# Kernel optimization log

Measured on AMD Instinct MI355X. Metric: run time of the kernel, lower is better.

## Reference

```python
import jax, jax.numpy as jnp
import numpy as np

DIM = 1024
HEADS = 16
DIM_HEAD = 64
SCALE = DIM_HEAD ** -0.5
LN_EPS = 1e-5


def layer_norm(x, g, b):
    mu = jnp.mean(x, axis=-1, keepdims=True)
    var = jnp.mean(jnp.square(x - mu), axis=-1, keepdims=True)
    return (x - mu) * jax.lax.rsqrt(var + LN_EPS) * g + b


def setup_inputs() -> dict:
    key = jax.random.key(0)
    ks = jax.random.split(key, 8)
    w_std = DIM ** -0.5  # keep GEMM outputs O(1)
    return {
        "query": jax.random.normal(ks[0], (4, 512, DIM), jnp.float32),
        "kv": jax.random.normal(ks[1], (4, 2048, DIM), jnp.float32),
        "ln_q_g": jnp.ones((DIM,), jnp.float32),
        "ln_q_b": jnp.zeros((DIM,), jnp.float32),
        "ln_kv_g": jnp.ones((DIM,), jnp.float32),
        "ln_kv_b": jnp.zeros((DIM,), jnp.float32),
        "Wq": jax.random.normal(ks[2], (DIM, DIM), jnp.float32) * w_std,
        "bq": jnp.zeros((DIM,), jnp.float32),
        "Wk": jax.random.normal(ks[3], (DIM, DIM), jnp.float32) * w_std,
        "bk": jnp.zeros((DIM,), jnp.float32),
        "Wv": jax.random.normal(ks[4], (DIM, DIM), jnp.float32) * w_std,
        "bv": jnp.zeros((DIM,), jnp.float32),
        "Wo": jax.random.normal(ks[5], (DIM, DIM), jnp.float32) * w_std,
        "bo": jnp.zeros((DIM,), jnp.float32),
    }


def reference(query, kv, ln_q_g, ln_q_b, ln_kv_g, ln_kv_b,
              Wq, bq, Wk, bk, Wv, bv, Wo, bo):
    kv_n = layer_norm(kv, ln_kv_g, ln_kv_b)            # (b, n_kv, d)
    residual = query
    q_n = layer_norm(query, ln_q_g, ln_q_b)            # (b, n_q, d)

    q = q_n @ Wq + bq                                   # (b, n_q, inner)
    kv_input = jnp.concatenate((kv_n, q_n), axis=-2)    # (b, n_kv+n_q, d)
    k = kv_input @ Wk + bk
    v = kv_input @ Wv + bv

    def split_heads(t):
        b, n, _ = t.shape
        return t.reshape(b, n, HEADS, DIM_HEAD).transpose(0, 2, 1, 3)  # b h n dh

    q = split_heads(q) * SCALE
    k = split_heads(k)
    v = split_heads(v)

    sim = jnp.einsum('bhid,bhjd->bhij', q, k)           # (b, h, n_q, n_kv+n_q)
    sim = sim - jax.lax.stop_gradient(jnp.max(sim, axis=-1, keepdims=True))
    attn = jax.nn.softmax(sim, axis=-1)
    out = jnp.einsum('bhij,bhjd->bhid', attn, v)        # (b, h, n_q, dh)

    b, h, n, dh = out.shape
    out = out.transpose(0, 2, 1, 3).reshape(b, n, h * dh)
    return out @ Wo + bo + residual
```

## Files before the change

### kernel.cpp

```cpp
#include <hip/hip_runtime.h>
#include <hip/hip_bf16.h>

#define B_    4
#define NQ    512
#define NKV   2048
#define NT    2560
#define DIM_  1024
#define HEADS 16
#define DH    64
#define NSEQT 10240
#define SCALE_Q_L2E 0.18033688011112042f

typedef short bf16x8 __attribute__((ext_vector_type(8)));
typedef float f32x4  __attribute__((ext_vector_type(4)));
typedef __hip_bfloat16 bf16;

__device__ inline void gll16(const bf16* g, bf16* l) {
  __builtin_amdgcn_global_load_lds(
      (const __attribute__((address_space(1))) unsigned int*)g,
      (__attribute__((address_space(3))) unsigned int*)l, 16, 0, 0);
}

__global__ __launch_bounds__(256) void ln_kernel(
    const float* __restrict__ query, const float* __restrict__ kv,
    const float* __restrict__ gq, const float* __restrict__ bq,
    const float* __restrict__ gkv, const float* __restrict__ bkv,
    bf16* __restrict__ X)
{
  int row = blockIdx.x;
  int b = row / NT, r = row % NT;
  const float *src, *g, *bb;
  if (r < NKV) { src = kv    + ((size_t)b*NKV + r)*DIM_;        g = gkv; bb = bkv; }
  else         { src = query + ((size_t)b*NQ + (r-NKV))*DIM_;   g = gq;  bb = bq;  }
  int t = threadIdx.x;
  float4 v = ((const float4*)src)[t];
  float s  = v.x+v.y+v.z+v.w;
  float s2 = v.x*v.x+v.y*v.y+v.z*v.z+v.w*v.w;
  #pragma unroll
  for (int m=1;m<64;m<<=1){ s += __shfl_xor(s,m,64); s2 += __shfl_xor(s2,m,64); }
  __shared__ float sh[8];
  int wave=t>>6, lane=t&63;
  if(lane==0){ sh[wave]=s; sh[4+wave]=s2; }
  __syncthreads();
  s  = sh[0]+sh[1]+sh[2]+sh[3];
  s2 = sh[4]+sh[5]+sh[6]+sh[7];
  float mu = s*(1.0f/DIM_);
  float rs = rsqrtf(s2*(1.0f/DIM_) - mu*mu + 1e-5f);
  float4 gg = ((const float4*)g)[t];
  float4 b4 = ((const float4*)bb)[t];
  bf16* dst = X + (size_t)row*DIM_ + t*4;
  dst[0]=__float2bfloat16((v.x-mu)*rs*gg.x + b4.x);
  dst[1]=__float2bfloat16((v.y-mu)*rs*gg.y + b4.y);
  dst[2]=__float2bfloat16((v.z-mu)*rs*gg.z + b4.z);
  dst[3]=__float2bfloat16((v.w-mu)*rs*gg.w + b4.w);
}

__global__ __launch_bounds__(256) void trw4_kernel(
    const float* __restrict__ W0, const float* __restrict__ W1,
    const float* __restrict__ W2, const float* __restrict__ W3,
    bf16* __restrict__ T0, bf16* __restrict__ T1,
    bf16* __restrict__ T2, bf16* __restrict__ T3)
{
  const float* W; bf16* Wt;
  switch (blockIdx.z) {
    case 0: W=W0; Wt=T0; break;
    case 1: W=W1; Wt=T1; break;
    case 2: W=W2; Wt=T2; break;
    default: W=W3; Wt=T3; break;
  }
  __shared__ __align__(16) bf16 Ws[64*72];
  int t = threadIdx.x;
  int k0 = blockIdx.x*64, n0 = blockIdx.y*64;
  int kr = t>>2, nseg = (t&3)*16;
  const float4* s4 = (const float4*)(W + (size_t)(k0+kr)*DIM_ + n0 + nseg);
  union { uint4 u[2]; bf16 h[16]; } pk;
  #pragma unroll
  for (int j=0;j<4;j++){
    float4 v = s4[j];
    pk.h[j*4+0]=__float2bfloat16(v.x); pk.h[j*4+1]=__float2bfloat16(v.y);
    pk.h[j*4+2]=__float2bfloat16(v.z); pk.h[j*4+3]=__float2bfloat16(v.w);
  }
  *(uint4*)(Ws + kr*72 + nseg)     = pk.u[0];
  *(uint4*)(Ws + kr*72 + nseg + 8) = pk.u[1];
  __syncthreads();
  int n = t&63, kseg = t>>6;
  union { uint4 u[2]; bf16 h[16]; } o;
  #pragma unroll
  for (int k=0;k<16;k++) o.h[k] = Ws[(kseg*16+k)*72 + n];
  bf16* dst = Wt + (size_t)(n0+n)*DIM_ + k0 + kseg*16;
  *(uint4*)dst = o.u[0];
  *(uint4*)(dst+8) = o.u[1];
}

template<int MODE>
__global__ __launch_bounds__(256) void gemm128(
    const bf16* __restrict__ A, const bf16* __restrict__ Wt,
    const float* __restrict__ bias, const float* __restrict__ residual,
    void* __restrict__ outv, int rows_per_batch, int row_offset,
    int a_batch_stride_rows, int n_seq, float scale)
{
  __shared__ __align__(16) char smem[32768];
  bf16* As = (bf16*)smem;
  bf16* Bs = (bf16*)(smem + 16384);
  float* Ts = (float*)smem;

  const int t = threadIdx.x;
  const int m0 = blockIdx.x*128, n0 = blockIdx.y*128;

  const int srow = t>>3;
  const int c = (t&7) ^ (srow&7);
  const bf16* aptr[4];
  const bf16* bptr[4];
  #pragma unroll
  for (int j=0;j<4;j++){
    int r = j*32 + srow;
    int gm = m0 + r;
    int bb = gm / rows_per_batch;
    aptr[j] = A + ((size_t)bb*a_batch_stride_rows + row_offset + (gm - bb*rows_per_batch))*(size_t)DIM_ + c*8;
    bptr[j] = Wt + (size_t)(n0 + r)*DIM_ + c*8;
  }
  bf16* lA = As + t*8;
  bf16* lB = Bs + t*8;

  const int wave = t>>6, lane = t&63, qq = lane>>4, mr = lane&15;
  const int wm = (wave>>1)*64, wn = (wave&1)*64;
  const int sw = mr&7;

  f32x4 acc[4][4] = {};
  for (int k0 = 0; k0 < DIM_; k0 += 64) {
    #pragma unroll
    for (int j=0;j<4;j++){
      gll16(aptr[j] + k0, lA + j*2048);
      gll16(bptr[j] + k0, lB + j*2048);
    }
    __syncthreads();
    #pragma unroll
    for (int ko=0; ko<2; ko++){
      const int slot = ((ko*4 + qq) ^ sw) * 8;
      bf16x8 af[4], bfr[4];
      #pragma unroll
      for (int ms=0;ms<4;ms++) af[ms]  = *(const bf16x8*)(As + (wm+ms*16+mr)*64 + slot);
      #pragma unroll
      for (int ns=0;ns<4;ns++) bfr[ns] = *(const bf16x8*)(Bs + (wn+ns*16+mr)*64 + slot);
      #pragma unroll
      for (int ms=0;ms<4;ms++)
        #pragma unroll
        for (int ns=0;ns<4;ns++)
          acc[ms][ns] = __builtin_amdgcn_mfma_f32_16x16x32_bf16(af[ms], bfr[ns], acc[ms][ns], 0,0,0);
    }
    __syncthreads();
  }

  const int lr = t>>3;
  const int cs = (t&7)*16;
  const int wlr = (wave>>1)*16 + qq*4;
  #pragma unroll
  for (int ms=0; ms<4; ms++){
    __syncthreads();
    #pragma unroll
    for (int ns=0; ns<4; ns++){
      int col = wn + ns*16 + mr;
      #pragma unroll
      for (int r=0;r<4;r++)
        Ts[(wlr+r)*132 + col] = acc[ms][ns][r];
    }
    __syncthreads();
    float v[16];
    #pragma unroll
    for (int j=0;j<4;j++){
      float4 f = *(const float4*)(Ts + lr*132 + cs + j*4);
      v[j*4+0]=f.x; v[j*4+1]=f.y; v[j*4+2]=f.z; v[j*4+3]=f.w;
    }
    int gr = m0 + (lr>>4)*64 + ms*16 + (lr&15);
    int gc = n0 + cs;
    if (MODE == 0) {
      float* out = (float*)outv;
      size_t base = (size_t)gr*DIM_ + gc;
      #pragma unroll
      for (int j=0;j<4;j++){
        float4 bv = *(const float4*)(bias + gc + j*4);
        float4 rv = *(const float4*)(residual + base + j*4);
        float4 o4;
        o4.x = v[j*4+0] + bv.x + rv.x;
        o4.y = v[j*4+1] + bv.y + rv.y;
        o4.z = v[j*4+2] + bv.z + rv.z;
        o4.w = v[j*4+3] + bv.w + rv.w;
        *(float4*)(out + base + j*4) = o4;
      }
    } else if (MODE == 1) {
      int bb = gr / rows_per_batch;
      int n  = gr - bb*rows_per_batch;
      int hh = gc>>6, dh = gc&63;
      bf16* out = (bf16*)outv + ((size_t)(bb*HEADS + hh)*n_seq + n)*DH + dh;
      union { uint4 u[2]; bf16 h[16]; } pk;
      #pragma unroll
      for (int j=0;j<16;j++) pk.h[j] = __float2bfloat16((v[j] + bias[gc+j])*scale);
      *(uint4*)out     = pk.u[0];
      *(uint4*)(out+8) = pk.u[1];
    } else {
      float bc = bias[gr];
      bf16* out = (bf16*)outv + (size_t)gr*NSEQT + gc;
      union { uint4 u[2]; bf16 h[16]; } pk;
      #pragma unroll
      for (int j=0;j<16;j++) pk.h[j] = __float2bfloat16(v[j] + bc);
      *(uint4*)out     = pk.u[0];
      *(uint4*)(out+8) = pk.u[1];
    }
  }
}

__global__ __launch_bounds__(256) void attn5_kernel(
    const bf16* __restrict__ Qh, const bf16* __restrict__ Kh,
    const bf16* __restrict__ VTg, bf16* __restrict__ Ctx)
{
  __shared__ __align__(16) bf16 KV[2][8192];
  __shared__ __align__(16) unsigned int Ps[4][576];

  const int t = threadIdx.x, wave = t>>6, lane = t&63;
  const int qq = lane>>4, mr = lane&15;
  const int blk = blockIdx.x;
  const int bh = (blk&7)*8 + (blk>>6);
  const int q0 = ((blk>>3)&7)*64;
  const int b = bh>>4, h = bh&15;

  const int sl = t>>2, sc = t&3;
  const int skey = ((sl&15)<<2) | (sl>>4);
  const bf16* Kb  = Kh + (size_t)bh*NT*DH + (size_t)skey*DH + sc*8;
  const bf16* VbT = VTg + ((size_t)(h*DH) + sl)*NSEQT + (size_t)b*NT + sc*8;

  const bf16* Qb = Qh + ((size_t)bh*NQ + q0 + wave*16 + mr)*DH;
  bf16x8 qf0 = *(const bf16x8*)(Qb + qq*8);
  bf16x8 qf1 = *(const bf16x8*)(Qb + 32 + qq*8);

  f32x4 o[4] = {};
  float l[4] = {};
  unsigned int* Pw = &Ps[wave][0];

  {
    bf16* bp = &KV[0][0];
    gll16(Kb,            bp + t*8);
    gll16(Kb + 32,       bp + 2048 + t*8);
    gll16(VbT,           bp + 4096 + t*8);
    gll16(VbT + 32,      bp + 6144 + t*8);
  }

  for (int it = 0; it < NT/64; it++) {
    __syncthreads();
    if (it + 1 < NT/64) {
      int kt = (it+1)*64;
      bf16* bp = &KV[(it+1)&1][0];
      gll16(Kb  + (size_t)kt*DH, bp + t*8);
      gll16(Kb  + (size_t)kt*DH + 32, bp + 2048 + t*8);
      gll16(VbT + kt,      bp + 4096 + t*8);
      gll16(VbT + kt + 32, bp + 6144 + t*8);
    }
    const bf16* cbuf = &KV[it&1][0];

    bf16x8 kl[4], kh_[4];
    #pragma unroll
    for (int g=0; g<4; g++){
      kl[g]  = *(const bf16x8*)(cbuf + ((g*16+mr)*32 + qq*8));
      kh_[g] = *(const bf16x8*)(cbuf + 2048 + ((g*16+mr)*32 + qq*8));
    }
    f32x4 s[4];
    #pragma unroll
    for (int g=0; g<4; g++){
      f32x4 z = {};
      z = __builtin_amdgcn_mfma_f32_16x16x32_bf16(qf0, kl[g],  z, 0,0,0);
      z = __builtin_amdgcn_mfma_f32_16x16x32_bf16(qf1, kh_[g], z, 0,0,0);
      s[g] = z;
    }
    bf16x8 vl[4], vh[4];
    #pragma unroll
    for (int n2=0; n2<4; n2++){
      vl[n2] = *(const bf16x8*)(cbuf + 4096 + ((n2*16+mr)*32 + qq*8));
      vh[n2] = *(const bf16x8*)(cbuf + 6144 + ((n2*16+mr)*32 + qq*8));
    }
    #pragma unroll
    for (int r=0; r<4; r++){
      float e0 = __builtin_amdgcn_exp2f(s[0][r]);
      float e1 = __builtin_amdgcn_exp2f(s[1][r]);
      float e2 = __builtin_amdgcn_exp2f(s[2][r]);
      float e3 = __builtin_amdgcn_exp2f(s[3][r]);
      l[r] += (e0+e1)+(e2+e3);
      unsigned a0 = __float_as_uint(e0) + 0x8000u;
      unsigned a1 = __float_as_uint(e1) + 0x8000u;
      unsigned a2 = __float_as_uint(e2) + 0x8000u;
      unsigned a3 = __float_as_uint(e3) + 0x8000u;
      uint2 w;
      w.x = __builtin_amdgcn_perm(a1, a0, 0x07060302u);
      w.y = __builtin_amdgcn_perm(a3, a2, 0x07060302u);
      *(uint2*)(Pw + (qq*4+r)*36 + mr*2) = w;
    }
    asm volatile("s_waitcnt lgkmcnt(0)" ::: "memory");
    bf16x8 plo = *(const bf16x8*)(Pw + mr*36 + qq*4);
    bf16x8 phi = *(const bf16x8*)(Pw + mr*36 + qq*4 + 16);
    #pragma unroll
    for (int n2=0; n2<4; n2++){
      o[n2] = __builtin_amdgcn_mfma_f32_16x16x32_bf16(plo, vl[n2], o[n2], 0,0,0);
      o[n2] = __builtin_amdgcn_mfma_f32_16x16x32_bf16(phi, vh[n2], o[n2], 0,0,0);
    }
  }

  float rl[4];
  #pragma unroll
  for (int r=0; r<4; r++){
    float v = l[r];
    #pragma unroll
    for (int m=1;m<16;m<<=1) v += __shfl_xor(v, m, 16);
    rl[r] = 1.0f / v;
  }

  __syncthreads();
  float* OfW = (float*)(&KV[0][0]) + wave*1088;
  #pragma unroll
  for (int n2=0; n2<4; n2++)
    #pragma unroll
    for (int r=0; r<4; r++)
      OfW[(qq*4+r)*68 + n2*16 + mr] = o[n2][r]*rl[r];
  asm volatile("s_waitcnt lgkmcnt(0)" ::: "memory");
  {
    int row = lane>>2, seg = (lane&3)*16;
    union { uint4 u[2]; bf16 hh[16]; } pkv;
    #pragma unroll
    for (int j=0;j<16;j++) pkv.hh[j] = __float2bfloat16(OfW[row*68 + seg + j]);
    bf16* dst = Ctx + ((size_t)b*NQ + q0 + wave*16 + row)*DIM_ + h*DH + seg;
    *(uint4*)dst = pkv.u[0];
    *(uint4*)(dst+8) = pkv.u[1];
  }
}

extern "C" void kernel_launch(void* const* d_in, const int* in_sizes, int n_in,
                              void* d_out, int out_size, void* d_ws, size_t ws_size,
                              hipStream_t stream)
{
  const float* query  = (const float*)d_in[0];
  const float* kv     = (const float*)d_in[1];
  const float* ln_q_g = (const float*)d_in[2];
  const float* ln_q_b = (const float*)d_in[3];
  const float* ln_kv_g= (const float*)d_in[4];
  const float* ln_kv_b= (const float*)d_in[5];
  const float* Wq = (const float*)d_in[6];
  const float* bq = (const float*)d_in[7];
  const float* Wk = (const float*)d_in[8];
  const float* bk = (const float*)d_in[9];
  const float* Wv = (const float*)d_in[10];
  const float* bv = (const float*)d_in[11];
  const float* Wo = (const float*)d_in[12];
  const float* bo = (const float*)d_in[13];
  float* out = (float*)d_out;

  char* ws = (char*)d_ws;
  size_t off = 0;
  auto take = [&](size_t bytes)->char* {
    char* p = ws + off; off += (bytes + 255) & ~(size_t)255; return p;
  };
  bf16* X    = (bf16*)take((size_t)B_*NT*DIM_*2);
  bf16* Qhb  = (bf16*)take((size_t)B_*NQ*DIM_*2);
  bf16* Khb  = (bf16*)take((size_t)B_*NT*DIM_*2);
  bf16* VTg  = (bf16*)take((size_t)DIM_*NSEQT*2);
  bf16* Ctx  = (bf16*)take((size_t)B_*NQ*DIM_*2);
  bf16* WtQ  = (bf16*)take((size_t)DIM_*DIM_*2);
  bf16* WtK  = (bf16*)take((size_t)DIM_*DIM_*2);
  bf16* WtV  = (bf16*)take((size_t)DIM_*DIM_*2);
  bf16* WtO  = (bf16*)take((size_t)DIM_*DIM_*2);

  trw4_kernel<<<dim3(16,16,4), 256, 0, stream>>>(Wq, Wk, Wv, Wo,
                                                 WtQ, WtK, WtV, WtO);

  ln_kernel<<<B_*NT, 256, 0, stream>>>(query, kv, ln_q_g, ln_q_b,
                                       ln_kv_g, ln_kv_b, X);

  gemm128<1><<<dim3(16,8), 256, 0, stream>>>(X, WtQ, bq, nullptr, Qhb,
                                             NQ, NKV, NT, NQ, SCALE_Q_L2E);
  gemm128<1><<<dim3(80,8), 256, 0, stream>>>(X, WtK, bk, nullptr, Khb,
                                             NT, 0, NT, NT, 1.0f);
  gemm128<2><<<dim3(8,80), 256, 0, stream>>>(WtV, X, bv, nullptr, VTg,
                                             DIM_, 0, DIM_, NSEQT, 1.0f);

  attn5_kernel<<<512, 256, 0, stream>>>(Qhb, Khb, VTg, Ctx);

  gemm128<0><<<dim3(16,8), 256, 0, stream>>>(Ctx, WtO, bo, query, out,
                                             NQ, 0, NQ, NQ, 1.0f);
}
```

Before: 285.1 us.

## Merge LN/transpose and QKV GEMMs into single launches with smaller K tile

Combines the layernorm and weight-transpose kernels into one prep launch, and the Q, K and V projection GEMMs into one grid-partitioned launch, to cut launch count and let the three GEMMs fill the GPU together. The GEMM core shrinks its K step from 64 to 32 (16 KB LDS instead of 32 KB) and drops the XOR swizzle, which may raise occupancy. In exchange it adds more barriers per K, possible LDS bank conflicts, and a runtime emode branch in place of a template.

```diff
diff --git a/kernel.cpp b/kernel.cpp
--- a/kernel.cpp
+++ b/kernel.cpp
@@ -21,148 +21,137 @@
       (__attribute__((address_space(3))) unsigned int*)l, 16, 0, 0);
 }
 
-__global__ __launch_bounds__(256) void ln_kernel(
+__global__ __launch_bounds__(256) void prep_kernel(
     const float* __restrict__ query, const float* __restrict__ kv,
-    const float* __restrict__ gq, const float* __restrict__ bq,
-    const float* __restrict__ gkv, const float* __restrict__ bkv,
-    bf16* __restrict__ X)
-{
-  int row = blockIdx.x;
-  int b = row / NT, r = row % NT;
-  const float *src, *g, *bb;
-  if (r < NKV) { src = kv    + ((size_t)b*NKV + r)*DIM_;        g = gkv; bb = bkv; }
-  else         { src = query + ((size_t)b*NQ + (r-NKV))*DIM_;   g = gq;  bb = bq;  }
-  int t = threadIdx.x;
-  float4 v = ((const float4*)src)[t];
-  float s  = v.x+v.y+v.z+v.w;
-  float s2 = v.x*v.x+v.y*v.y+v.z*v.z+v.w*v.w;
-  #pragma unroll
-  for (int m=1;m<64;m<<=1){ s += __shfl_xor(s,m,64); s2 += __shfl_xor(s2,m,64); }
-  __shared__ float sh[8];
-  int wave=t>>6, lane=t&63;
-  if(lane==0){ sh[wave]=s; sh[4+wave]=s2; }
-  __syncthreads();
-  s  = sh[0]+sh[1]+sh[2]+sh[3];
-  s2 = sh[4]+sh[5]+sh[6]+sh[7];
-  float mu = s*(1.0f/DIM_);
-  float rs = rsqrtf(s2*(1.0f/DIM_) - mu*mu + 1e-5f);
-  float4 gg = ((const float4*)g)[t];
-  float4 b4 = ((const float4*)bb)[t];
-  bf16* dst = X + (size_t)row*DIM_ + t*4;
-  dst[0]=__float2bfloat16((v.x-mu)*rs*gg.x + b4.x);
-  dst[1]=__float2bfloat16((v.y-mu)*rs*gg.y + b4.y);
-  dst[2]=__float2bfloat16((v.z-mu)*rs*gg.z + b4.z);
-  dst[3]=__float2bfloat16((v.w-mu)*rs*gg.w + b4.w);
-}
-
-__global__ __launch_bounds__(256) void trw4_kernel(
+    const float* __restrict__ lgq, const float* __restrict__ lbq,
+    const float* __restrict__ lgkv, const float* __restrict__ lbkv,
+    bf16* __restrict__ X,
     const float* __restrict__ W0, const float* __restrict__ W1,
     const float* __restrict__ W2, const float* __restrict__ W3,
     bf16* __restrict__ T0, bf16* __restrict__ T1,
     bf16* __restrict__ T2, bf16* __restrict__ T3)
 {
-  const float* W; bf16* Wt;
-  switch (blockIdx.z) {
-    case 0: W=W0; Wt=T0; break;
-    case 1: W=W1; Wt=T1; break;
-    case 2: W=W2; Wt=T2; break;
-    default: W=W3; Wt=T3; break;
-  }
-  __shared__ __align__(16) bf16 Ws[64*72];
-  int t = threadIdx.x;
-  int k0 = blockIdx.x*64, n0 = blockIdx.y*64;
-  int kr = t>>2, nseg = (t&3)*16;
-  const float4* s4 = (const float4*)(W + (size_t)(k0+kr)*DIM_ + n0 + nseg);
-  union { uint4 u[2]; bf16 h[16]; } pk;
-  #pragma unroll
-  for (int j=0;j<4;j++){
-    float4 v = s4[j];
-    pk.h[j*4+0]=__float2bfloat16(v.x); pk.h[j*4+1]=__float2bfloat16(v.y);
-    pk.h[j*4+2]=__float2bfloat16(v.z); pk.h[j*4+3]=__float2bfloat16(v.w);
-  }
-  *(uint4*)(Ws + kr*72 + nseg)     = pk.u[0];
-  *(uint4*)(Ws + kr*72 + nseg + 8) = pk.u[1];
-  __syncthreads();
-  int n = t&63, kseg = t>>6;
-  union { uint4 u[2]; bf16 h[16]; } o;
-  #pragma unroll
-  for (int k=0;k<16;k++) o.h[k] = Ws[(kseg*16+k)*72 + n];
-  bf16* dst = Wt + (size_t)(n0+n)*DIM_ + k0 + kseg*16;
-  *(uint4*)dst = o.u[0];
-  *(uint4*)(dst+8) = o.u[1];
-}
-
-template<int MODE>
-__global__ __launch_bounds__(256) void gemm128(
-    const bf16* __restrict__ A, const bf16* __restrict__ Wt,
+  __shared__ __align__(16) char psm[9216];
+  const int t = threadIdx.x;
+  const int blkid = blockIdx.x;
+  if (blkid < B_*NT) {
+    float* sh = (float*)psm;
+    int b = blkid / NT, r = blkid % NT;
+    const float *src, *g, *bb;
+    if (r < NKV) { src = kv    + ((size_t)b*NKV + r)*DIM_;      g = lgkv; bb = lbkv; }
+    else         { src = query + ((size_t)b*NQ + (r-NKV))*DIM_; g = lgq;  bb = lbq;  }
+    float4 v = ((const float4*)src)[t];
+    float s  = v.x+v.y+v.z+v.w;
+    float s2 = v.x*v.x+v.y*v.y+v.z*v.z+v.w*v.w;
+    #pragma unroll
+    for (int m=1;m<64;m<<=1){ s += __shfl_xor(s,m,64); s2 += __shfl_xor(s2,m,64); }
+    int wave=t>>6, lane=t&63;
+    if(lane==0){ sh[wave]=s; sh[4+wave]=s2; }
+    __syncthreads();
+    s  = sh[0]+sh[1]+sh[2]+sh[3];
+    s2 = sh[4]+sh[5]+sh[6]+sh[7];
+    float mu = s*(1.0f/DIM_);
+    float rs = rsqrtf(s2*(1.0f/DIM_) - mu*mu + 1e-5f);
+    float4 gg = ((const float4*)g)[t];
+    float4 b4 = ((const float4*)bb)[t];
+    bf16* dst = X + (size_t)blkid*DIM_ + t*4;
+    dst[0]=__float2bfloat16((v.x-mu)*rs*gg.x + b4.x);
+    dst[1]=__float2bfloat16((v.y-mu)*rs*gg.y + b4.y);
+    dst[2]=__float2bfloat16((v.z-mu)*rs*gg.z + b4.z);
+    dst[3]=__float2bfloat16((v.w-mu)*rs*gg.w + b4.w);
+  } else {
+    int l = blkid - B_*NT;
+    const float* W; bf16* Wt;
+    switch (l>>8) {
+      case 0: W=W0; Wt=T0; break;
+      case 1: W=W1; Wt=T1; break;
+      case 2: W=W2; Wt=T2; break;
+      default: W=W3; Wt=T3; break;
+    }
+    int rem = l & 255;
+    int k0 = (rem&15)*64, n0 = (rem>>4)*64;
+    bf16* Ws = (bf16*)psm;
+    int kr = t>>2, nseg = (t&3)*16;
+    const float4* s4 = (const float4*)(W + (size_t)(k0+kr)*DIM_ + n0 + nseg);
+    union { uint4 u[2]; bf16 h[16]; } pk;
+    #pragma unroll
+    for (int j=0;j<4;j++){
+      float4 v = s4[j];
+      pk.h[j*4+0]=__float2bfloat16(v.x); pk.h[j*4+1]=__float2bfloat16(v.y);
+      pk.h[j*4+2]=__float2bfloat16(v.z); pk.h[j*4+3]=__float2bfloat16(v.w);
+    }
+    *(uint4*)(Ws + kr*72 + nseg)     = pk.u[0];
+    *(uint4*)(Ws + kr*72 + nseg + 8) = pk.u[1];
+    __syncthreads();
+    int n = t&63, kseg = t>>6;
+    union { uint4 u[2]; bf16 h[16]; } o;
+    #pragma unroll
+    for (int k=0;k<16;k++) o.h[k] = Ws[(kseg*16+k)*72 + n];
+    bf16* dst = Wt + (size_t)(n0+n)*DIM_ + k0 + kseg*16;
+    *(uint4*)dst = o.u[0];
+    *(uint4*)(dst+8) = o.u[1];
+  }
+}
+
+__device__ __forceinline__ void gemm_core(
+    const bf16* __restrict__ A, const bf16* __restrict__ Bmat,
     const float* __restrict__ bias, const float* __restrict__ residual,
     void* __restrict__ outv, int rows_per_batch, int row_offset,
-    int a_batch_stride_rows, int n_seq, float scale)
-{
-  __shared__ __align__(16) char smem[32768];
+    int a_batch_stride_rows, int n_seq, float scale,
+    int emode, int m0, int n0, char* smem)
+{
   bf16* As = (bf16*)smem;
-  bf16* Bs = (bf16*)(smem + 16384);
+  bf16* Bs = (bf16*)(smem + 8192);
   float* Ts = (float*)smem;
 
   const int t = threadIdx.x;
-  const int m0 = blockIdx.x*128, n0 = blockIdx.y*128;
-
-  const int srow = t>>3;
-  const int c = (t&7) ^ (srow&7);
-  const bf16* aptr[4];
-  const bf16* bptr[4];
-  #pragma unroll
-  for (int j=0;j<4;j++){
-    int r = j*32 + srow;
-    int gm = m0 + r;
-    int bb = gm / rows_per_batch;
-    aptr[j] = A + ((size_t)bb*a_batch_stride_rows + row_offset + (gm - bb*rows_per_batch))*(size_t)DIM_ + c*8;
-    bptr[j] = Wt + (size_t)(n0 + r)*DIM_ + c*8;
-  }
-  bf16* lA = As + t*8;
-  bf16* lB = Bs + t*8;
+  const int r0 = t>>2, c8 = (t&3)*8;
+  int gm0 = m0 + r0, gm1 = m0 + 64 + r0;
+  int b0i = gm0 / rows_per_batch, b1i = gm1 / rows_per_batch;
+  const bf16* a0 = A + ((size_t)b0i*a_batch_stride_rows + row_offset + (gm0 - b0i*rows_per_batch))*(size_t)DIM_ + c8;
+  const bf16* a1 = A + ((size_t)b1i*a_batch_stride_rows + row_offset + (gm1 - b1i*rows_per_batch))*(size_t)DIM_ + c8;
+  const bf16* wb0 = Bmat + (size_t)(n0 + r0)*DIM_ + c8;
+  const bf16* wb1 = Bmat + (size_t)(n0 + 64 + r0)*DIM_ + c8;
+  bf16* lA0 = As + t*8;  bf16* lA1 = As + 64*32 + t*8;
+  bf16* lB0 = Bs + t*8;  bf16* lB1 = Bs + 64*32 + t*8;
 
   const int wave = t>>6, lane = t&63, qq = lane>>4, mr = lane&15;
   const int wm = (wave>>1)*64, wn = (wave&1)*64;
-  const int sw = mr&7;
 
   f32x4 acc[4][4] = {};
-  for (int k0 = 0; k0 < DIM_; k0 += 64) {
-    #pragma unroll
-    for (int j=0;j<4;j++){
-      gll16(aptr[j] + k0, lA + j*2048);
-      gll16(bptr[j] + k0, lB + j*2048);
-    }
-    __syncthreads();
-    #pragma unroll
-    for (int ko=0; ko<2; ko++){
-      const int slot = ((ko*4 + qq) ^ sw) * 8;
-      bf16x8 af[4], bfr[4];
+  for (int k0 = 0; k0 < DIM_; k0 += 32) {
+    gll16(a0 + k0, lA0);
+    gll16(a1 + k0, lA1);
+    gll16(wb0 + k0, lB0);
+    gll16(wb1 + k0, lB1);
+    __syncthreads();
+    bf16x8 af[4], bfr[4];
+    #pragma unroll
+    for (int ms=0;ms<4;ms++) af[ms]  = *(const bf16x8*)(As + (wm+ms*16+mr)*32 + qq*8);
+    #pragma unroll
+    for (int ns=0;ns<4;ns++) bfr[ns] = *(const bf16x8*)(Bs + (wn+ns*16+mr)*32 + qq*8);
+    #pragma unroll
+    for (int ms=0;ms<4;ms++)
       #pragma unroll
-      for (int ms=0;ms<4;ms++) af[ms]  = *(const bf16x8*)(As + (wm+ms*16+mr)*64 + slot);
+      for (int ns=0;ns<4;ns++)
+        acc[ms][ns] = __builtin_amdgcn_mfma_f32_16x16x32_bf16(af[ms], bfr[ns], acc[ms][ns], 0,0,0);
+    __syncthreads();
+  }
+
+  const int lr = t>>3, cs = (t&7)*16;
+  for (int R=0; R<4; R++){
+    if ((wave>>1) == (R>>1)) {
       #pragma unroll
-      for (int ns=0;ns<4;ns++) bfr[ns] = *(const bf16x8*)(Bs + (wn+ns*16+mr)*64 + slot);
-      #pragma unroll
-      for (int ms=0;ms<4;ms++)
+      for (int ms2=0; ms2<2; ms2++){
+        int ms = (R&1)*2 + ms2;
         #pragma unroll
-        for (int ns=0;ns<4;ns++)
-          acc[ms][ns] = __builtin_amdgcn_mfma_f32_16x16x32_bf16(af[ms], bfr[ns], acc[ms][ns], 0,0,0);
-    }
-    __syncthreads();
-  }
-
-  const int lr = t>>3;
-  const int cs = (t&7)*16;
-  const int wlr = (wave>>1)*16 + qq*4;
-  #pragma unroll
-  for (int ms=0; ms<4; ms++){
-    __syncthreads();
-    #pragma unroll
-    for (int ns=0; ns<4; ns++){
-      int col = wn + ns*16 + mr;
-      #pragma unroll
-      for (int r=0;r<4;r++)
-        Ts[(wlr+r)*132 + col] = acc[ms][ns][r];
+        for (int ns=0; ns<4; ns++){
+          int col = wn + ns*16 + mr;
+          #pragma unroll
+          for (int r=0;r<4;r++)
+            Ts[(ms2*16 + qq*4 + r)*132 + col] = acc[ms][ns][r];
+        }
+      }
     }
     __syncthreads();
     float v[16];
@@ -171,9 +160,9 @@
       float4 f = *(const float4*)(Ts + lr*132 + cs + j*4);
       v[j*4+0]=f.x; v[j*4+1]=f.y; v[j*4+2]=f.z; v[j*4+3]=f.w;
     }
-    int gr = m0 + (lr>>4)*64 + ms*16 + (lr&15);
+    int gr = m0 + R*32 + lr;
     int gc = n0 + cs;
-    if (MODE == 0) {
+    if (emode == 0) {
       float* out = (float*)outv;
       size_t base = (size_t)gr*DIM_ + gc;
       #pragma unroll
@@ -187,7 +176,7 @@
         o4.w = v[j*4+3] + bv.w + rv.w;
         *(float4*)(out + base + j*4) = o4;
       }
-    } else if (MODE == 1) {
+    } else if (emode == 1) {
       int bb = gr / rows_per_batch;
       int n  = gr - bb*rows_per_batch;
       int hh = gc>>6, dh = gc&63;
@@ -206,7 +195,43 @@
       *(uint4*)out     = pk.u[0];
       *(uint4*)(out+8) = pk.u[1];
     }
-  }
+    __syncthreads();
+  }
+}
+
+__global__ __launch_bounds__(256) void gemm_qkv(
+    const bf16* __restrict__ X,
+    const bf16* __restrict__ WtQ, const bf16* __restrict__ WtK,
+    const bf16* __restrict__ WtV,
+    const float* __restrict__ bq, const float* __restrict__ bk,
+    const float* __restrict__ bv,
+    bf16* __restrict__ Qhb, bf16* __restrict__ Khb, bf16* __restrict__ VTg)
+{
+  __shared__ __align__(16) char smem[16896];
+  const int blk = blockIdx.x;
+  if (blk < 128) {
+    gemm_core(X, WtQ, bq, nullptr, Qhb, NQ, NKV, NT, NQ, SCALE_Q_L2E, 1,
+              (blk&15)*128, (blk>>4)*128, smem);
+  } else if (blk < 768) {
+    int l = blk - 128;
+    gemm_core(X, WtK, bk, nullptr, Khb, NT, 0, NT, NT, 1.0f, 1,
+              (l%80)*128, (l/80)*128, smem);
+  } else {
+    int l = blk - 768;
+    gemm_core(WtV, X, bv, nullptr, VTg, DIM_, 0, DIM_, NSEQT, 1.0f, 2,
+              (l&7)*128, (l>>3)*128, smem);
+  }
+}
+
+__global__ __launch_bounds__(256) void gemm_o(
+    const bf16* __restrict__ Ctx, const bf16* __restrict__ WtO,
+    const float* __restrict__ bo, const float* __restrict__ residual,
+    float* __restrict__ out)
+{
+  __shared__ __align__(16) char smem[16896];
+  const int blk = blockIdx.x;
+  gemm_core(Ctx, WtO, bo, residual, out, B_*NQ, 0, B_*NQ, NQ, 1.0f, 0,
+            (blk&15)*128, (blk>>4)*128, smem);
 }
 
 __global__ __launch_bounds__(256) void attn5_kernel(
@@ -365,21 +390,14 @@
   bf16* WtV  = (bf16*)take((size_t)DIM_*DIM_*2);
   bf16* WtO  = (bf16*)take((size_t)DIM_*DIM_*2);
 
-  trw4_kernel<<<dim3(16,16,4), 256, 0, stream>>>(Wq, Wk, Wv, Wo,
-                                                 WtQ, WtK, WtV, WtO);
-
-  ln_kernel<<<B_*NT, 256, 0, stream>>>(query, kv, ln_q_g, ln_q_b,
-                                       ln_kv_g, ln_kv_b, X);
-
-  gemm128<1><<<dim3(16,8), 256, 0, stream>>>(X, WtQ, bq, nullptr, Qhb,
-                                             NQ, NKV, NT, NQ, SCALE_Q_L2E);
-  gemm128<1><<<dim3(80,8), 256, 0, stream>>>(X, WtK, bk, nullptr, Khb,
-                                             NT, 0, NT, NT, 1.0f);
-  gemm128<2><<<dim3(8,80), 256, 0, stream>>>(WtV, X, bv, nullptr, VTg,
-                                             DIM_, 0, DIM_, NSEQT, 1.0f);
+  prep_kernel<<<B_*NT + 1024, 256, 0, stream>>>(
+      query, kv, ln_q_g, ln_q_b, ln_kv_g, ln_kv_b, X,
+      Wq, Wk, Wv, Wo, WtQ, WtK, WtV, WtO);
+
+  gemm_qkv<<<1408, 256, 0, stream>>>(X, WtQ, WtK, WtV, bq, bk, bv,
+                                     Qhb, Khb, VTg);
 
   attn5_kernel<<<512, 256, 0, stream>>>(Qhb, Khb, VTg, Ctx);
 
-  gemm128<0><<<dim3(16,8), 256, 0, stream>>>(Ctx, WtO, bo, query, out,
-                                             NQ, 0, NQ, NQ, 1.0f);
-}
+  gemm_o<<<128, 256, 0, stream>>>(Ctx, WtO, bo, query, out);
+}
```

Result: faster. 271.9 us (-4.6%).
